# Performance work log

Hardware: AMD Instinct MI355X
Metric: run time of the kernel (lower is better)

Reference implementation:

```python
import jax, jax.numpy as jnp
import numpy as np

D_MODEL = 1024
NHEAD = 16
DIM_HEAD = D_MODEL // NHEAD  # 64
SCALE = DIM_HEAD ** -0.5


def _rope_freqs():
    # freqs list = 10000^(-i/32) for i in 0..31 (len == dim_head//2), then cat [f, -f]
    half = 10000.0 ** (-jnp.arange(DIM_HEAD // 2, dtype=jnp.float32) / (DIM_HEAD // 2))
    return jnp.concatenate([half, -half], axis=0)  # [dim_head]


def _rotate_half(t):
    t1, t2 = jnp.split(t, 2, axis=-1)
    return jnp.concatenate([t2, t1], axis=-1)


def setup_inputs() -> dict:
    key = jax.random.key(0)
    ks = jax.random.split(key, 6)
    B, S = 4, 2048
    x = jax.random.normal(ks[0], (B, S, D_MODEL), dtype=jnp.float32)
    p = jnp.broadcast_to(jnp.arange(S, dtype=jnp.int32), (B, S))
    lim_qkv = (1.0 / D_MODEL) ** 0.5
    Wqkv_w = jax.random.uniform(ks[1], (3 * D_MODEL, D_MODEL), jnp.float32, -lim_qkv, lim_qkv)
    Wqkv_b = jax.random.uniform(ks[2], (3 * D_MODEL,), jnp.float32, -lim_qkv, lim_qkv)
    Wo_w = jax.random.uniform(ks[3], (D_MODEL, D_MODEL), jnp.float32, -lim_qkv, lim_qkv)
    Wo_b = jax.random.uniform(ks[4], (D_MODEL,), jnp.float32, -lim_qkv, lim_qkv)
    return {"x": x, "p": p, "Wqkv_w": Wqkv_w, "Wqkv_b": Wqkv_b, "Wo_w": Wo_w, "Wo_b": Wo_b}


def reference(x, p, Wqkv_w, Wqkv_b, Wo_w, Wo_b):
    B, S, D = x.shape
    qkv = (x @ Wqkv_w.T + Wqkv_b).reshape(B, S, 3, NHEAD, DIM_HEAD)
    # torch: transpose(3,1) -> (B, H, 3, S, Dh), unbind dim=2
    q = jnp.transpose(qkv[:, :, 0], (0, 2, 1, 3))  # [B,H,S,Dh]
    k = jnp.transpose(qkv[:, :, 1], (0, 2, 1, 3))
    v = jnp.transpose(qkv[:, :, 2], (0, 2, 1, 3))
    freqs = _rope_freqs()
    ang = p[..., None].astype(jnp.float32) * freqs  # [B,S,Dh]
    cos = jnp.cos(ang)[:, None]  # [B,1,S,Dh] broadcasts over heads
    sin = jnp.sin(ang)[:, None]
    q = q * cos + _rotate_half(q) * sin
    k = k * cos + _rotate_half(k) * sin
    scores = jnp.einsum("bhqd,bhkd->bhqk", q, k) * SCALE
    attn = jax.nn.softmax(scores, axis=-1)
    out = jnp.einsum("bhqk,bhkd->bhqd", attn, v)
    out = jnp.transpose(out, (0, 2, 1, 3)).reshape(B, S, D)
    return out @ Wo_w.T + Wo_b
```

## Files before the change

kernel.cpp:

```cpp
#include <hip/hip_runtime.h>
#include <hip/hip_bf16.h>
#include <cmath>

constexpr int D_MODEL = 1024;
constexpr int NHEAD   = 16;
constexpr int DH      = 64;
constexpr int BATCH   = 4;
constexpr int SEQ     = 2048;
constexpr int TOKENS  = BATCH * SEQ;
constexpr float SCALE = 0.125f;
constexpr float QSF   = 0.125f * 1.44269504088896340736f;

typedef __attribute__((ext_vector_type(8))) short bf16x8;
typedef __attribute__((ext_vector_type(4))) short short4v;
typedef __attribute__((ext_vector_type(4))) float f32x4;

__device__ inline short f2bf(float f) {
    union { float f; unsigned u; } v; v.f = f;
    unsigned r = v.u + 0x7FFFu + ((v.u >> 16) & 1u);
    return (short)(r >> 16);
}
__device__ inline float bf2f(short s) {
    union { float f; unsigned u; } v;
    v.u = ((unsigned)(unsigned short)s) << 16;
    return v.f;
}
__device__ inline void llds16(const void* g, void* l) {
    __builtin_amdgcn_global_load_lds(
        (const __attribute__((address_space(1))) unsigned*)g,
        (__attribute__((address_space(3))) unsigned*)l, 16, 0, 0);
}

__global__ __launch_bounds__(256) void cvt_bf16_kernel(
    const float* __restrict__ src, short* __restrict__ dst, int n8)
{
    int i = blockIdx.x * blockDim.x + threadIdx.x;
    if (i >= n8) return;
    const float4* s = (const float4*)src + (size_t)i * 2;
    float4 a = s[0], b = s[1];
    bf16x8 v;
    v[0] = f2bf(a.x); v[1] = f2bf(a.y); v[2] = f2bf(a.z); v[3] = f2bf(a.w);
    v[4] = f2bf(b.x); v[5] = f2bf(b.y); v[6] = f2bf(b.z); v[7] = f2bf(b.w);
    *(bf16x8*)(dst + (size_t)i * 8) = v;
}

template<int OUT_BF16>
__global__ __launch_bounds__(256) void gemm_mfma_kernel(
    const short* __restrict__ A, const short* __restrict__ B,
    const float* __restrict__ bias, void* __restrict__ C,
    int M, int N, int K)
{
    __shared__ short As[128 * 64];
    __shared__ short Bs[128 * 64];
    const int tid  = threadIdx.x;
    const int w    = tid >> 6;
    const int lane = tid & 63;
    const int q16  = lane & 15;
    const int quad = lane >> 4;
    const int wm   = (w & 1) * 64;
    const int wn   = (w >> 1) * 64;
    const int bm   = blockIdx.x * 128;
    const int bn   = blockIdx.y * 128;

    const int srow = w * 32 + (lane >> 3);
    const int kcs  = lane & 7;

    f32x4 acc[4][4];
    #pragma unroll
    for (int i = 0; i < 4; i++)
        #pragma unroll
        for (int j = 0; j < 4; j++) acc[i][j] = (f32x4){0.f, 0.f, 0.f, 0.f};

    for (int k0 = 0; k0 < K; k0 += 64) {
        __syncthreads();
        #pragma unroll
        for (int i = 0; i < 4; i++) {
            int row = srow + i * 8;
            int kc  = kcs ^ (row & 7);
            const short* ga = A + (size_t)(bm + row) * K + k0 + kc * 8;
            const short* gb = B + (size_t)(bn + row) * K + k0 + kc * 8;
            short* la = &As[(w * 32 + i * 8) * 64];
            short* lb = &Bs[(w * 32 + i * 8) * 64];
            llds16(ga, la);
            llds16(gb, lb);
        }
        __syncthreads();
        #pragma unroll
        for (int ks = 0; ks < 2; ks++) {
            bf16x8 af[4], bfr[4];
            #pragma unroll
            for (int t = 0; t < 4; t++) {
                int ra = wm + t * 16 + q16;
                int ca = (ks * 4 + quad) ^ (ra & 7);
                af[t]  = *(const bf16x8*)&As[ra * 64 + ca * 8];
                int rb = wn + t * 16 + q16;
                int cb = (ks * 4 + quad) ^ (rb & 7);
                bfr[t] = *(const bf16x8*)&Bs[rb * 64 + cb * 8];
            }
            #pragma unroll
            for (int mb = 0; mb < 4; mb++)
                #pragma unroll
                for (int nb = 0; nb < 4; nb++)
                    acc[mb][nb] = __builtin_amdgcn_mfma_f32_16x16x32_bf16(
                        af[mb], bfr[nb], acc[mb][nb], 0, 0, 0);
        }
    }

    #pragma unroll
    for (int nb = 0; nb < 4; nb++) {
        const int cn = bn + wn + nb * 16 + q16;
        const float bv = bias[cn];
        #pragma unroll
        for (int mb = 0; mb < 4; mb++) {
            const int rm = bm + wm + mb * 16 + quad * 4;
            #pragma unroll
            for (int r = 0; r < 4; r++) {
                float v = acc[mb][nb][r] + bv;
                if (OUT_BF16)
                    ((short*)C)[(size_t)(rm + r) * N + cn] = f2bf(v);
                else
                    ((float*)C)[(size_t)(rm + r) * N + cn] = v;
            }
        }
    }
}

__global__ __launch_bounds__(256) void rope_bf16_kernel(
    short* __restrict__ qkv, const int* __restrict__ p)
{
    int idx = blockIdx.x * blockDim.x + threadIdx.x;
    int i   = idx & 31;
    int h   = (idx >> 5) & 15;
    int tok = idx >> 9;
    if (tok >= TOKENS) return;
    float freq = powf(10000.f, -(float)i * (1.f / 32.f));
    float ang  = (float)p[tok] * freq;
    float sn, c;
    sincosf(ang, &sn, &c);
    short* base = qkv + (size_t)tok * 3072 + h * 64 + i;
    float q1 = bf2f(base[0]),    q2 = bf2f(base[32]);
    base[0]    = f2bf(fmaf(q1, c,  q2 * sn) * QSF);
    base[32]   = f2bf(fmaf(q2, c, -q1 * sn) * QSF);
    float k1 = bf2f(base[1024]), k2 = bf2f(base[1056]);
    base[1024] = f2bf(fmaf(k1, c,  k2 * sn));
    base[1056] = f2bf(fmaf(k2, c, -k1 * sn));
}

__global__ __launch_bounds__(256, 2) void attn_mfma_kernel(
    const short* __restrict__ qkv, short* __restrict__ out)
{
    __shared__ short Ks[64 * 64];
    __shared__ short VsT[64][72];
    __shared__ short Ps[4][16][72];

    const int tid  = threadIdx.x;
    const int w    = tid >> 6;
    const int lane = tid & 63;
    const int q16  = lane & 15;
    const int quad = lane >> 4;
    const int gid  = blockIdx.x;
    const int bh   = gid & 63;
    const int qblk = gid >> 6;
    const int b    = bh >> 4;
    const int h    = bh & 15;
    const int qtok0 = qblk * 256 + w * 64;

    bf16x8 qf[4][2];
    #pragma unroll
    for (int qb = 0; qb < 4; qb++) {
        const short* Qrow =
            qkv + (size_t)(b * SEQ + qtok0 + qb * 16 + q16) * 3072 + h * 64;
        qf[qb][0] = *(const bf16x8*)(Qrow + quad * 8);
        qf[qb][1] = *(const bf16x8*)(Qrow + 32 + quad * 8);
    }

    f32x4 o[4][4];
    #pragma unroll
    for (int qb = 0; qb < 4; qb++)
        #pragma unroll
        for (int md = 0; md < 4; md++) o[qb][md] = (f32x4){0.f, 0.f, 0.f, 0.f};
    float lsum[4] = {0.f, 0.f, 0.f, 0.f};

    const short* Kg = qkv + (size_t)b * SEQ * 3072 + 1024 + h * 64;
    const short* Vg = Kg + 1024;

    const int krow = w * 16 + (lane >> 3);
    const int kc   = (lane & 7) ^ (krow & 7);
    short* kdst0 = &Ks[(w * 16) * 64];
    short* kdst1 = &Ks[(w * 16 + 8) * 64];
    const int vkey = (tid & 31) * 2;
    const int vdb  = (tid >> 5) * 8;

    for (int kt = 0; kt < SEQ; kt += 64) {
        __syncthreads();
        llds16(Kg + (size_t)(kt + krow) * 3072 + kc * 8, kdst0);
        llds16(Kg + (size_t)(kt + krow + 8) * 3072 + kc * 8, kdst1);
        {
            const short* vsrc = Vg + (size_t)(kt + vkey) * 3072 + vdb;
            uint4 a  = *(const uint4*)vsrc;
            uint4 bb = *(const uint4*)(vsrc + 3072);
            *(unsigned*)&VsT[vdb + 0][vkey] = __builtin_amdgcn_perm(bb.x, a.x, 0x05040100);
            *(unsigned*)&VsT[vdb + 1][vkey] = __builtin_amdgcn_perm(bb.x, a.x, 0x07060302);
            *(unsigned*)&VsT[vdb + 2][vkey] = __builtin_amdgcn_perm(bb.y, a.y, 0x05040100);
            *(unsigned*)&VsT[vdb + 3][vkey] = __builtin_amdgcn_perm(bb.y, a.y, 0x07060302);
            *(unsigned*)&VsT[vdb + 4][vkey] = __builtin_amdgcn_perm(bb.z, a.z, 0x05040100);
            *(unsigned*)&VsT[vdb + 5][vkey] = __builtin_amdgcn_perm(bb.z, a.z, 0x07060302);
            *(unsigned*)&VsT[vdb + 6][vkey] = __builtin_amdgcn_perm(bb.w, a.w, 0x05040100);
            *(unsigned*)&VsT[vdb + 7][vkey] = __builtin_amdgcn_perm(bb.w, a.w, 0x07060302);
        }
        __syncthreads();

        bf16x8 af[4][2], av[4][2];
        #pragma unroll
        for (int mb = 0; mb < 4; mb++) {
            #pragma unroll
            for (int ks = 0; ks < 2; ks++) {
                int c = ((ks * 4 + quad) ^ (q16 & 7)) * 8;
                af[mb][ks] = *(const bf16x8*)&Ks[(mb * 16 + q16) * 64 + c];
                av[mb][ks] = *(const bf16x8*)&VsT[mb * 16 + q16][ks * 32 + quad * 8];
            }
        }

        #pragma unroll
        for (int qb = 0; qb < 4; qb++) {
            f32x4 sc[4];
            #pragma unroll
            for (int mb = 0; mb < 4; mb++) {
                f32x4 c = {0.f, 0.f, 0.f, 0.f};
                c = __builtin_amdgcn_mfma_f32_16x16x32_bf16(af[mb][0], qf[qb][0], c, 0, 0, 0);
                c = __builtin_amdgcn_mfma_f32_16x16x32_bf16(af[mb][1], qf[qb][1], c, 0, 0, 0);
                sc[mb] = c;
            }
            float ltile = 0.f;
            #pragma unroll
            for (int mb = 0; mb < 4; mb++) {
                float p0 = __builtin_amdgcn_exp2f(sc[mb][0]);
                float p1 = __builtin_amdgcn_exp2f(sc[mb][1]);
                float p2 = __builtin_amdgcn_exp2f(sc[mb][2]);
                float p3 = __builtin_amdgcn_exp2f(sc[mb][3]);
                ltile += (p0 + p1) + (p2 + p3);
                unsigned u0 = __float_as_uint(p0) + 0x8000u;
                unsigned u1 = __float_as_uint(p1) + 0x8000u;
                unsigned u2 = __float_as_uint(p2) + 0x8000u;
                unsigned u3 = __float_as_uint(p3) + 0x8000u;
                uint2 pk;
                pk.x = __builtin_amdgcn_perm(u1, u0, 0x07060302);
                pk.y = __builtin_amdgcn_perm(u3, u2, 0x07060302);
                *(uint2*)&Ps[w][q16][mb * 16 + quad * 4] = pk;
            }
            lsum[qb] += ltile;
            #pragma unroll
            for (int ks = 0; ks < 2; ks++) {
                bf16x8 pb = *(const bf16x8*)&Ps[w][q16][ks * 32 + quad * 8];
                #pragma unroll
                for (int md = 0; md < 4; md++)
                    o[qb][md] = __builtin_amdgcn_mfma_f32_16x16x32_bf16(
                        av[md][ks], pb, o[qb][md], 0, 0, 0);
            }
        }
    }

    #pragma unroll
    for (int qb = 0; qb < 4; qb++) {
        float l = lsum[qb];
        l += __shfl_xor(l, 16);
        l += __shfl_xor(l, 32);
        float inv = 1.f / l;
        short* orow = out + (size_t)(b * SEQ + qtok0 + qb * 16 + q16) * 1024
                      + h * 64 + quad * 4;
        #pragma unroll
        for (int md = 0; md < 4; md++) {
            short4v t;
            t[0] = f2bf(o[qb][md][0] * inv);
            t[1] = f2bf(o[qb][md][1] * inv);
            t[2] = f2bf(o[qb][md][2] * inv);
            t[3] = f2bf(o[qb][md][3] * inv);
            *(short4v*)(orow + md * 16) = t;
        }
    }
}

extern "C" void kernel_launch(void* const* d_in, const int* in_sizes, int n_in,
                              void* d_out, int out_size, void* d_ws, size_t ws_size,
                              hipStream_t stream)
{
    (void)in_sizes; (void)n_in; (void)out_size; (void)ws_size;
    const float* x      = (const float*)d_in[0];
    const int*   p      = (const int*)  d_in[1];
    const float* Wqkv_w = (const float*)d_in[2];
    const float* Wqkv_b = (const float*)d_in[3];
    const float* Wo_w   = (const float*)d_in[4];
    const float* Wo_b   = (const float*)d_in[5];
    float* out = (float*)d_out;

    short* xb     = (short*)d_ws;
    short* wqkvb  = xb + (size_t)TOKENS * 1024;
    short* wob    = wqkvb + (size_t)3072 * 1024;
    short* qkvb   = wob + (size_t)1024 * 1024;
    short* attnob = qkvb + (size_t)TOKENS * 3072;

    dim3 blk(256);

    cvt_bf16_kernel<<<dim3(TOKENS * 1024 / 8 / 256), blk, 0, stream>>>(x, xb, TOKENS * 1024 / 8);
    cvt_bf16_kernel<<<dim3(3072 * 1024 / 8 / 256), blk, 0, stream>>>(Wqkv_w, wqkvb, 3072 * 1024 / 8);
    cvt_bf16_kernel<<<dim3(1024 * 1024 / 8 / 256), blk, 0, stream>>>(Wo_w, wob, 1024 * 1024 / 8);

    gemm_mfma_kernel<1><<<dim3(TOKENS / 128, 3072 / 128), blk, 0, stream>>>(
        xb, wqkvb, Wqkv_b, qkvb, TOKENS, 3072, 1024);

    rope_bf16_kernel<<<dim3(TOKENS * NHEAD * 32 / 256), blk, 0, stream>>>(qkvb, p);

    attn_mfma_kernel<<<dim3(512), blk, 0, stream>>>(qkvb, attnob);

    gemm_mfma_kernel<0><<<dim3(TOKENS / 128, 1024 / 128), blk, 0, stream>>>(
        attnob, wob, Wo_b, out, TOKENS, 1024, 1024);
}
```

Measured before the change: 299.9 us.

## Double-buffer K/V tiles in attention, fuse convert kernels, and use fast RoPE trig

The attention kernel now double-buffers the K and V shared-memory tiles. It prefetches the next tile's K through direct global-to-LDS loads and V into registers while the current tile is computed, and drops to one barrier per iteration. V is stored in a swizzled 64x64 layout instead of a padded transpose, and the P-tile MFMAs are split so the first half starts before the second half's exponentials are done. The three fp32-to-bf16 conversion launches are merged into one, and RoPE uses hardware exp2/sin/cos on a range-reduced angle instead of powf/sincosf, which may cost some accuracy. The prefetch adds registers and doubles the LDS footprint, which could reduce occupancy.

```diff
diff --git a/kernel.cpp b/kernel.cpp
--- a/kernel.cpp
+++ b/kernel.cpp
@@ -31,17 +31,26 @@
         (__attribute__((address_space(3))) unsigned*)l, 16, 0, 0);
 }
 
-__global__ __launch_bounds__(256) void cvt_bf16_kernel(
-    const float* __restrict__ src, short* __restrict__ dst, int n8)
+constexpr int N8_X    = TOKENS * 1024 / 8;
+constexpr int N8_WQKV = 3072 * 1024 / 8;
+constexpr int N8_WO   = 1024 * 1024 / 8;
+
+__global__ __launch_bounds__(256) void cvt3_bf16_kernel(
+    const float* __restrict__ sx, const float* __restrict__ sq,
+    const float* __restrict__ so,
+    short* __restrict__ dx, short* __restrict__ dq, short* __restrict__ dо_)
 {
     int i = blockIdx.x * blockDim.x + threadIdx.x;
-    if (i >= n8) return;
-    const float4* s = (const float4*)src + (size_t)i * 2;
+    const float* src; short* dst; int off;
+    if (i < N8_X)                  { src = sx; dst = dx;  off = i; }
+    else if (i < N8_X + N8_WQKV)   { src = sq; dst = dq;  off = i - N8_X; }
+    else                           { src = so; dst = dо_; off = i - N8_X - N8_WQKV; }
+    const float4* s = (const float4*)src + (size_t)off * 2;
     float4 a = s[0], b = s[1];
     bf16x8 v;
     v[0] = f2bf(a.x); v[1] = f2bf(a.y); v[2] = f2bf(a.z); v[3] = f2bf(a.w);
     v[4] = f2bf(b.x); v[5] = f2bf(b.y); v[6] = f2bf(b.z); v[7] = f2bf(b.w);
-    *(bf16x8*)(dst + (size_t)i * 8) = v;
+    *(bf16x8*)(dst + (size_t)off * 8) = v;
 }
 
 template<int OUT_BF16>
@@ -133,10 +142,12 @@
     int h   = (idx >> 5) & 15;
     int tok = idx >> 9;
     if (tok >= TOKENS) return;
-    float freq = powf(10000.f, -(float)i * (1.f / 32.f));
-    float ang  = (float)p[tok] * freq;
-    float sn, c;
-    sincosf(ang, &sn, &c);
+    float frev = __builtin_amdgcn_exp2f((float)i * -0.4152410118609203f)
+                 * 0.15915494309189535f;
+    float t = (float)p[tok] * frev;
+    t -= floorf(t);
+    float sn = __builtin_amdgcn_sinf(t);
+    float c  = __builtin_amdgcn_cosf(t);
     short* base = qkv + (size_t)tok * 3072 + h * 64 + i;
     float q1 = bf2f(base[0]),    q2 = bf2f(base[32]);
     base[0]    = f2bf(fmaf(q1, c,  q2 * sn) * QSF);
@@ -149,8 +160,8 @@
 __global__ __launch_bounds__(256, 2) void attn_mfma_kernel(
     const short* __restrict__ qkv, short* __restrict__ out)
 {
-    __shared__ short Ks[64 * 64];
-    __shared__ short VsT[64][72];
+    __shared__ short Ks[2][64 * 64];
+    __shared__ short Vs[2][64 * 64];
     __shared__ short Ps[4][16][72];
 
     const int tid  = threadIdx.x;
@@ -186,38 +197,52 @@
 
     const int krow = w * 16 + (lane >> 3);
     const int kc   = (lane & 7) ^ (krow & 7);
-    short* kdst0 = &Ks[(w * 16) * 64];
-    short* kdst1 = &Ks[(w * 16 + 8) * 64];
     const int vkey = (tid & 31) * 2;
     const int vdb  = (tid >> 5) * 8;
 
-    for (int kt = 0; kt < SEQ; kt += 64) {
-        __syncthreads();
-        llds16(Kg + (size_t)(kt + krow) * 3072 + kc * 8, kdst0);
-        llds16(Kg + (size_t)(kt + krow + 8) * 3072 + kc * 8, kdst1);
-        {
-            const short* vsrc = Vg + (size_t)(kt + vkey) * 3072 + vdb;
-            uint4 a  = *(const uint4*)vsrc;
-            uint4 bb = *(const uint4*)(vsrc + 3072);
-            *(unsigned*)&VsT[vdb + 0][vkey] = __builtin_amdgcn_perm(bb.x, a.x, 0x05040100);
-            *(unsigned*)&VsT[vdb + 1][vkey] = __builtin_amdgcn_perm(bb.x, a.x, 0x07060302);
-            *(unsigned*)&VsT[vdb + 2][vkey] = __builtin_amdgcn_perm(bb.y, a.y, 0x05040100);
-            *(unsigned*)&VsT[vdb + 3][vkey] = __builtin_amdgcn_perm(bb.y, a.y, 0x07060302);
-            *(unsigned*)&VsT[vdb + 4][vkey] = __builtin_amdgcn_perm(bb.z, a.z, 0x05040100);
-            *(unsigned*)&VsT[vdb + 5][vkey] = __builtin_amdgcn_perm(bb.z, a.z, 0x07060302);
-            *(unsigned*)&VsT[vdb + 6][vkey] = __builtin_amdgcn_perm(bb.w, a.w, 0x05040100);
-            *(unsigned*)&VsT[vdb + 7][vkey] = __builtin_amdgcn_perm(bb.w, a.w, 0x07060302);
-        }
-        __syncthreads();
+    auto vwrite = [&](int buf, const uint4& a, const uint4& bb) {
+        #pragma unroll
+        for (int j = 0; j < 8; j++) {
+            unsigned lo = (j & 1) ? 0x07060302u : 0x05040100u;
+            unsigned sa = (&a.x)[j >> 1], sb = (&bb.x)[j >> 1];
+            *(unsigned*)&Vs[buf][(vdb + j) * 64 + (((vkey >> 3) ^ j) << 3) + (vkey & 7)] =
+                __builtin_amdgcn_perm(sb, sa, lo);
+        }
+    };
+
+    {
+        llds16(Kg + (size_t)krow * 3072 + kc * 8, &Ks[0][(w * 16) * 64]);
+        llds16(Kg + (size_t)(krow + 8) * 3072 + kc * 8, &Ks[0][(w * 16 + 8) * 64]);
+        const short* vsrc = Vg + (size_t)vkey * 3072 + vdb;
+        uint4 a  = *(const uint4*)vsrc;
+        uint4 bb = *(const uint4*)(vsrc + 3072);
+        vwrite(0, a, bb);
+    }
+    __syncthreads();
+
+    int cur = 0;
+    for (int t = 0; t < SEQ / 64; t++) {
+        uint4 pva, pvb;
+        const bool pf = (t < SEQ / 64 - 1);
+        if (pf) {
+            const int ktn = (t + 1) * 64;
+            llds16(Kg + (size_t)(ktn + krow) * 3072 + kc * 8,
+                   &Ks[cur ^ 1][(w * 16) * 64]);
+            llds16(Kg + (size_t)(ktn + krow + 8) * 3072 + kc * 8,
+                   &Ks[cur ^ 1][(w * 16 + 8) * 64]);
+            const short* vsrc = Vg + (size_t)(ktn + vkey) * 3072 + vdb;
+            pva = *(const uint4*)vsrc;
+            pvb = *(const uint4*)(vsrc + 3072);
+        }
 
         bf16x8 af[4][2], av[4][2];
         #pragma unroll
         for (int mb = 0; mb < 4; mb++) {
             #pragma unroll
             for (int ks = 0; ks < 2; ks++) {
-                int c = ((ks * 4 + quad) ^ (q16 & 7)) * 8;
-                af[mb][ks] = *(const bf16x8*)&Ks[(mb * 16 + q16) * 64 + c];
-                av[mb][ks] = *(const bf16x8*)&VsT[mb * 16 + q16][ks * 32 + quad * 8];
+                int c = (((ks * 4 + quad) ^ (q16 & 7))) * 8;
+                af[mb][ks] = *(const bf16x8*)&Ks[cur][(mb * 16 + q16) * 64 + c];
+                av[mb][ks] = *(const bf16x8*)&Vs[cur][(mb * 16 + q16) * 64 + c];
             }
         }
 
@@ -233,7 +258,7 @@
             }
             float ltile = 0.f;
             #pragma unroll
-            for (int mb = 0; mb < 4; mb++) {
+            for (int mb = 0; mb < 2; mb++) {
                 float p0 = __builtin_amdgcn_exp2f(sc[mb][0]);
                 float p1 = __builtin_amdgcn_exp2f(sc[mb][1]);
                 float p2 = __builtin_amdgcn_exp2f(sc[mb][2]);
@@ -248,16 +273,38 @@
                 pk.y = __builtin_amdgcn_perm(u3, u2, 0x07060302);
                 *(uint2*)&Ps[w][q16][mb * 16 + quad * 4] = pk;
             }
+            bf16x8 pb0 = *(const bf16x8*)&Ps[w][q16][quad * 8];
+            #pragma unroll
+            for (int mb = 2; mb < 4; mb++) {
+                float p0 = __builtin_amdgcn_exp2f(sc[mb][0]);
+                float p1 = __builtin_amdgcn_exp2f(sc[mb][1]);
+                float p2 = __builtin_amdgcn_exp2f(sc[mb][2]);
+                float p3 = __builtin_amdgcn_exp2f(sc[mb][3]);
+                ltile += (p0 + p1) + (p2 + p3);
+                unsigned u0 = __float_as_uint(p0) + 0x8000u;
+                unsigned u1 = __float_as_uint(p1) + 0x8000u;
+                unsigned u2 = __float_as_uint(p2) + 0x8000u;
+                unsigned u3 = __float_as_uint(p3) + 0x8000u;
+                uint2 pk;
+                pk.x = __builtin_amdgcn_perm(u1, u0, 0x07060302);
+                pk.y = __builtin_amdgcn_perm(u3, u2, 0x07060302);
+                *(uint2*)&Ps[w][q16][mb * 16 + quad * 4] = pk;
+            }
+            #pragma unroll
+            for (int md = 0; md < 4; md++)
+                o[qb][md] = __builtin_amdgcn_mfma_f32_16x16x32_bf16(
+                    av[md][0], pb0, o[qb][md], 0, 0, 0);
+            bf16x8 pb1 = *(const bf16x8*)&Ps[w][q16][32 + quad * 8];
+            #pragma unroll
+            for (int md = 0; md < 4; md++)
+                o[qb][md] = __builtin_amdgcn_mfma_f32_16x16x32_bf16(
+                    av[md][1], pb1, o[qb][md], 0, 0, 0);
             lsum[qb] += ltile;
-            #pragma unroll
-            for (int ks = 0; ks < 2; ks++) {
-                bf16x8 pb = *(const bf16x8*)&Ps[w][q16][ks * 32 + quad * 8];
-                #pragma unroll
-                for (int md = 0; md < 4; md++)
-                    o[qb][md] = __builtin_amdgcn_mfma_f32_16x16x32_bf16(
-                        av[md][ks], pb, o[qb][md], 0, 0, 0);
-            }
-        }
+        }
+
+        if (pf) vwrite(cur ^ 1, pva, pvb);
+        __syncthreads();
+        cur ^= 1;
     }
 
     #pragma unroll
@@ -301,9 +348,8 @@
 
     dim3 blk(256);
 
-    cvt_bf16_kernel<<<dim3(TOKENS * 1024 / 8 / 256), blk, 0, stream>>>(x, xb, TOKENS * 1024 / 8);
-    cvt_bf16_kernel<<<dim3(3072 * 1024 / 8 / 256), blk, 0, stream>>>(Wqkv_w, wqkvb, 3072 * 1024 / 8);
-    cvt_bf16_kernel<<<dim3(1024 * 1024 / 8 / 256), blk, 0, stream>>>(Wo_w, wob, 1024 * 1024 / 8);
+    cvt3_bf16_kernel<<<dim3((N8_X + N8_WQKV + N8_WO) / 256), blk, 0, stream>>>(
+        x, Wqkv_w, Wo_w, xb, wqkvb, wob);
 
     gemm_mfma_kernel<1><<<dim3(TOKENS / 128, 3072 / 128), blk, 0, stream>>>(
         xb, wqkvb, Wqkv_b, qkvb, TOKENS, 3072, 1024);
```

Result: faster. 282.5 us (-5.8%).
